# Kernel tuning notes

Hardware: AMD Instinct MI355X
Metric: run time of the kernel (lower is better)

## Reference

```python
import jax, jax.numpy as jnp
import numpy as np

N, G, MAX_N, E, H = 20000, 200, 100, 320000, 4
F_IN, NHID, NCLS = 128, 128, 10
DQ = 2 * NHID   # pooling-stack input dim = 2*nhid
K1 = 25         # ceil(0.25 * avg_num_nodes)


def _lin(key, fi, fo):
    kw, kb = jax.random.split(key)
    s = 1.0 / np.sqrt(fi)
    return (jax.random.uniform(kw, (fi, fo), jnp.float32, -s, s),
            jax.random.uniform(kb, (fo,), jnp.float32, -s, s))


def setup_inputs():
    key = jax.random.key(0)
    ks = jax.random.split(key, 32)
    x = jax.random.normal(ks[0], (N, F_IN), jnp.float32)
    gid = jax.random.randint(ks[1], (E,), 0, G)
    u = jax.random.randint(ks[2], (E,), 0, MAX_N)
    v = jax.random.randint(ks[3], (E,), 0, MAX_N)
    edge_index = jnp.stack([gid * MAX_N + u, gid * MAX_N + v]).astype(jnp.int32)
    batch = (jnp.arange(N) // MAX_N).astype(jnp.int32)
    d = {}
    d['x'], d['edge_index'], d['batch'] = x, edge_index, batch
    d['W1'], d['b1'] = _lin(ks[4], F_IN, NHID)
    d['W2'], d['b2'] = _lin(ks[5], NHID, NHID)
    d['S0'] = jax.random.normal(ks[6], (1, K1, DQ), jnp.float32) * (1.0 / np.sqrt(DQ))
    d['Wq0'], d['bq0'] = _lin(ks[7], DQ, DQ)
    d['Wk0'], d['bk0'] = _lin(ks[8], DQ, DQ)
    d['Wv0'], d['bv0'] = _lin(ks[9], DQ, DQ)
    d['Wo0'], d['bo0'] = _lin(ks[10], DQ, DQ)
    d['Wq1'], d['bq1'] = _lin(ks[11], DQ, NHID)
    d['Wk1'], d['bk1'] = _lin(ks[12], DQ, NHID)
    d['Wv1'], d['bv1'] = _lin(ks[13], DQ, NHID)
    d['Wo1'], d['bo1'] = _lin(ks[14], NHID, NHID)
    d['S2'] = jax.random.normal(ks[15], (1, 1, NHID), jnp.float32) * (1.0 / np.sqrt(NHID))
    d['Wq2'], d['bq2'] = _lin(ks[16], NHID, NHID)
    d['Wk2'], d['bk2'] = _lin(ks[17], NHID, NHID)
    d['Wv2'], d['bv2'] = _lin(ks[18], NHID, NHID)
    d['Wo2'], d['bo2'] = _lin(ks[19], NHID, NHID)
    d['Wl'], d['bl'] = _lin(ks[20], NHID, NHID)
    d['Wc1'], d['bc1'] = _lin(ks[21], NHID, NHID)
    d['Wc2'], d['bc2'] = _lin(ks[22], NHID, NHID // 2)
    d['Wc3'], d['bc3'] = _lin(ks[23], NHID // 2, NCLS)
    return d


def gcn(h, src, dst, W, b):
    # PyG GCNConv: add self loops, sym-normalize, scatter-add, bias
    h = h @ W
    loop = jnp.arange(N, dtype=src.dtype)
    s = jnp.concatenate([src, loop])
    t = jnp.concatenate([dst, loop])
    deg = jax.ops.segment_sum(jnp.ones(s.shape[0], h.dtype), t, num_segments=N)
    dinv = jax.lax.rsqrt(jnp.maximum(deg, 1.0))
    norm = (dinv[s] * dinv[t])[:, None]
    return jax.ops.segment_sum(h[s] * norm, t, num_segments=N) + b


def to_dense(v, batch):
    counts = jax.ops.segment_sum(jnp.ones(v.shape[0], jnp.int32), batch, num_segments=G)
    start = jnp.cumsum(counts) - counts
    pos = jnp.arange(v.shape[0]) - start[batch]
    dense = jnp.zeros((G, MAX_N, v.shape[1]), v.dtype).at[batch, pos].set(v)
    mask = jnp.zeros((G, MAX_N), bool).at[batch, pos].set(True)
    return dense, mask


def attn_block(Q, K, V, Wo, bo, mask_bias):
    # MAB core with cluster=True: softmax over the QUERY (seed) axis, ln=False
    B, nq, dv = Q.shape
    dh = dv // H
    Qh = Q.reshape(B, nq, H, dh)
    Kh = K.reshape(B, K.shape[1], H, dh)
    Vh = V.reshape(B, V.shape[1], H, dh)
    score = jnp.einsum('bqhd,bkhd->bhqk', Qh, Kh) / jnp.sqrt(jnp.float32(dv))
    if mask_bias is not None:
        score = score + mask_bias[:, None, None, :]
    A = jax.nn.softmax(score, axis=2)  # cluster assignment over seeds
    O = Q + jnp.einsum('bhqk,bkhd->bqhd', A, Vh).reshape(B, nq, dv)
    return O + jax.nn.relu(O @ Wo + bo)


def reference(x, edge_index, batch, W1, b1, W2, b2, S0, Wq0, bq0, Wk0, bk0, Wv0, bv0, Wo0, bo0,
              Wq1, bq1, Wk1, bk1, Wv1, bv1, Wo1, bo1, S2, Wq2, bq2, Wk2, bk2, Wv2, bv2, Wo2, bo2,
              Wl, bl, Wc1, bc1, Wc2, bc2, Wc3, bc3):
    src, dst = edge_index[0], edge_index[1]
    x1 = jax.nn.relu(gcn(x, src, dst, W1, b1))
    x2 = jax.nn.relu(gcn(x1, src, dst, W2, b2))
    p1 = jax.ops.segment_sum(x1, batch, num_segments=G)  # global_add_pool
    p2 = jax.ops.segment_sum(x2, batch, num_segments=G)
    xcat = jnp.concatenate([x1, x2], axis=1)             # [N, 2*nhid]
    dense, mask = to_dense(xcat, batch)
    mask_bias = (1.0 - mask.astype(jnp.float32)) * -1e9
    # --- GMPool_G: PMA with GCNConv for K/V on the node graph ---
    Kd, _ = to_dense(gcn(xcat, src, dst, Wk0, bk0), batch)
    Vd, _ = to_dense(gcn(xcat, src, dst, Wv0, bv0), batch)
    Q0 = jnp.broadcast_to(S0, (G, K1, DQ)) @ Wq0 + bq0
    O0 = attn_block(Q0, Kd, Vd, Wo0, bo0, mask_bias)     # [G, 25, 256]
    # --- SelfAtt (SAB), mask consumed above ---
    Q1 = O0 @ Wq1 + bq1
    K1d = O0 @ Wk1 + bk1
    V1d = O0 @ Wv1 + bv1
    O1 = attn_block(Q1, K1d, V1d, Wo1, bo1, None)        # [G, 25, 128]
    # --- GMPool_I: PMA with 1 seed ---
    Q2 = jnp.broadcast_to(S2, (G, 1, NHID)) @ Wq2 + bq2
    K2d = O1 @ Wk2 + bk2
    V2d = O1 @ Wv2 + bv2
    O2 = attn_block(Q2, K2d, V2d, Wo2, bo2, None)        # [G, 1, 128]
    z = (O2 @ Wl + bl)[:, 0, :]
    z = jax.nn.relu(z @ Wc1 + bc1)                        # dropout = identity at eval
    z = jax.nn.relu(z @ Wc2 + bc2)
    logits = z @ Wc3 + bc3
    return (logits, p1, p2)
```

## Files before the change

### kernel.cpp

```cpp
#include <hip/hip_runtime.h>
#include <hip/hip_bf16.h>
#include <cstdint>
#include <cstddef>

typedef __hip_bfloat16 bf16;
typedef __attribute__((ext_vector_type(8))) short s16x8;
typedef __attribute__((ext_vector_type(4))) float f32x4;

#define MAXN 100
#define HH   4
#define FIN  128
#define KS1  25

static inline int ceil_div(int a, int b){ return (a + b - 1) / b; }

__device__ inline short f2bf(float f){
  unsigned int u = __float_as_uint(f);
  u = (u + 0x7FFF + ((u >> 16) & 1)) >> 16;
  return (short)u;
}
__device__ inline float loadf(const void* s, int i, bool isbf){
  return isbf ? __bfloat162float(((const bf16*)s)[i]) : ((const float*)s)[i];
}
__device__ inline bool block_sniff(const void* x, int tid, int* flagS){
  if (tid < 64){
    unsigned short b = ((const unsigned short*)x)[2 * tid];
    float v = __uint_as_float(((unsigned)b) << 16);
    float a = fabsf(v);
    bool ok = (a >= 6.1e-5f && a <= 16384.f);
    unsigned long long m = __ballot(ok);
    if (tid == 0) *flagS = (__popcll(m) >= 32) ? 1 : 0;
  }
  __syncthreads();
  return *flagS != 0;
}

struct PrepBatch {
  const void* src[40];
  void*       dst[40];
  int         a[40];
  int         b[40];
  int         blk0[41];
  int         ne;
  const void* xptr;
};

__global__ __launch_bounds__(256) void prep_all(PrepBatch pb){
  __shared__ int flagS;
  int tid = threadIdx.x;
  bool isbf = block_sniff(pb.xptr, tid, &flagS);
  int blk = blockIdx.x;
  int t = 0;
  while (t + 1 < pb.ne && pb.blk0[t + 1] <= blk) t++;
  int local = blk - pb.blk0[t];
  const void* s = pb.src[t];
  int bt = pb.b[t];
  if (bt < 0){
    float val = (bt == -2) ? 1.0f : 0.0f;
    int n = pb.a[t];
    float* d = (float*)pb.dst[t];
    int v = local * 256 + tid;
    int base = v * 4;
    if (base + 3 < n) ((float4*)d)[v] = make_float4(val, val, val, val);
    else for (int j = base; j < n && j < base + 4; j++) d[j] = val;
  } else if (bt == 0){
    int n = pb.a[t];
    float* d = (float*)pb.dst[t];
    int v = local * 256 + tid;
    int base = v * 4;
    if (base + 3 < n){
      float4 f;
      if (isbf){
        ushort4 u = ((const ushort4*)s)[v];
        f.x = __uint_as_float(((unsigned)u.x) << 16);
        f.y = __uint_as_float(((unsigned)u.y) << 16);
        f.z = __uint_as_float(((unsigned)u.z) << 16);
        f.w = __uint_as_float(((unsigned)u.w) << 16);
      } else f = ((const float4*)s)[v];
      ((float4*)d)[v] = f;
    } else {
      for (int j = base; j < n && j < base + 4; j++) d[j] = loadf(s, j, isbf);
    }
  } else {
    int K = pb.a[t], Nn = bt, ldt = K + 8;
    short* d = (short*)pb.dst[t];
    int i = local * 256 + tid;
    if (i < K * Nn){
      int n = i / K, k = i - n * K;
      d[(size_t)n * ldt + k] = f2bf(loadf(s, (size_t)k * Nn + n, isbf));
    }
  }
}

__global__ __launch_bounds__(256) void adj_cnt(const int* __restrict__ src, const int* __restrict__ dst,
                                               float* __restrict__ A, int e){
  int i = blockIdx.x * 256 + threadIdx.x;
  if (i >= e) return;
  int s = src[i], d = dst[i];
  int g = d / MAXN;
  int dl = d - g * MAXN;
  int sl = s - (s / MAXN) * MAXN;
  atomicAdd(&A[(size_t)g * (MAXN * MAXN) + dl * MAXN + sl], 1.0f);
}

#define GLDK 136
__global__ __launch_bounds__(512) void gcn_all(
    const void* __restrict__ X,
    const float* __restrict__ Adj,
    const short* __restrict__ W1t, const float* __restrict__ b1,
    const short* __restrict__ W2t, const float* __restrict__ b2,
    short* __restrict__ xaggB,
    float* __restrict__ p1, float* __restrict__ p2)
{
  __shared__ short As[112 * GLDK];
  __shared__ short S1[112 * GLDK];
  __shared__ short S2[128 * GLDK];
  __shared__ short S4[128 * GLDK];
  __shared__ float dinvL[112];
  __shared__ int flagS;
  int g = blockIdx.x;
  int tid = threadIdx.x;
  bool isbf = block_sniff(X, tid, &flagS);
  int wave = tid >> 6, lane = tid & 63;
  int quad = lane >> 4, l16 = lane & 15;
  int gn = wave * 16 + l16;

  for (int i = tid; i < 112 * GLDK / 2; i += 512){ ((int*)As)[i] = 0; ((int*)S1)[i] = 0; }
  for (int i = tid; i < 128 * GLDK / 2; i += 512){ ((int*)S2)[i] = 0; ((int*)S4)[i] = 0; }

  const float* Ag = Adj + (size_t)g * (MAXN * MAXN);
  if (tid < 400){
    int r = tid >> 2, j0 = (tid & 3) * 25;
    const float* row = Ag + r * MAXN + j0;
    float s = 0.f;
#pragma unroll
    for (int j = 0; j < 25; j++) s += row[j];
    s += __shfl_xor(s, 1); s += __shfl_xor(s, 2);
    if ((tid & 3) == 0) dinvL[r] = rsqrtf(1.0f + s);
  }
  __syncthreads();

  for (int i = tid; i < MAXN * MAXN; i += 512){
    int r = i / MAXN, s = i - r * MAXN;
    float v = Ag[i] + (r == s ? 1.0f : 0.0f);
    As[r * GLDK + s] = f2bf(v * dinvL[r] * dinvL[s]);
  }
  for (int i = tid; i < MAXN * 16; i += 512){
    int r = i >> 4, k8 = (i & 15) << 3;
    s16x8 v;
    if (isbf){
      v = *reinterpret_cast<const s16x8*>((const short*)X + (size_t)(g * MAXN + r) * 128 + k8);
    } else {
      const float* ap = (const float*)X + (size_t)(g * MAXN + r) * 128 + k8;
      float4 f0 = *reinterpret_cast<const float4*>(ap);
      float4 f1 = *reinterpret_cast<const float4*>(ap + 4);
      v[0] = f2bf(f0.x); v[1] = f2bf(f0.y); v[2] = f2bf(f0.z); v[3] = f2bf(f0.w);
      v[4] = f2bf(f1.x); v[5] = f2bf(f1.y); v[6] = f2bf(f1.z); v[7] = f2bf(f1.w);
    }
    *reinterpret_cast<s16x8*>(&S1[r * GLDK + k8]) = v;
  }
  __syncthreads();

  f32x4 acc[7];
  auto zacc = [&](){
#pragma unroll
    for (int rt = 0; rt < 7; rt++) acc[rt] = (f32x4){0.f,0.f,0.f,0.f};
  };
  auto passL = [&](const short* Abuf, const short* Bbuf){
#pragma unroll
    for (int kt = 0; kt < 4; kt++){
      int kb = kt * 32 + quad * 8;
      s16x8 bf0 = *reinterpret_cast<const s16x8*>(&Bbuf[gn * GLDK + kb]);
#pragma unroll
      for (int rt = 0; rt < 7; rt++){
// ... 11 lines not shown
      for (int rt = 0; rt < 7; rt++){
        s16x8 a = *reinterpret_cast<const s16x8*>(&Abuf[(rt * 16 + l16) * GLDK + kb]);
        acc[rt] = __builtin_amdgcn_mfma_f32_16x16x32_bf16(a, bf0, acc[rt], 0, 0, 0);
      }
    }
  };
  auto writeB = [&](short* Bbuf){
#pragma unroll
    for (int rt = 0; rt < 7; rt++){
      short4 o;
      o.x = f2bf(acc[rt][0]); o.y = f2bf(acc[rt][1]);
      o.z = f2bf(acc[rt][2]); o.w = f2bf(acc[rt][3]);
      *reinterpret_cast<short4*>(&Bbuf[gn * GLDK + rt * 16 + quad * 4]) = o;
    }
  };

  float s1sum = 0.f, s2sum = 0.f;
  auto hopEpi = [&](const float* bias, short* AoutA, short* BoutB, float& sum){
    float bv = bias[gn];
#pragma unroll
    for (int rt = 0; rt < 7; rt++){
      float vals[4];
#pragma unroll
      for (int r = 0; r < 4; r++){
        int row = rt * 16 + quad * 4 + r;
        float v = fmaxf(acc[rt][r] + bv, 0.f);
        vals[r] = v;
        if (row < MAXN) sum += v;
      }
      short4 o;
      o.x = f2bf(vals[0]); o.y = f2bf(vals[1]); o.z = f2bf(vals[2]); o.w = f2bf(vals[3]);
      *reinterpret_cast<short4*>(&BoutB[gn * GLDK + rt * 16 + quad * 4]) = o;
      if (AoutA){
        AoutA[(rt * 16 + quad * 4 + 0) * GLDK + gn] = o.x;
        AoutA[(rt * 16 + quad * 4 + 1) * GLDK + gn] = o.y;
        AoutA[(rt * 16 + quad * 4 + 2) * GLDK + gn] = o.z;
        AoutA[(rt * 16 + quad * 4 + 3) * GLDK + gn] = o.w;
      }
    }
  };
  auto xaggEpi = [&](int colbase){
    int col = gn + colbase;
#pragma unroll
    for (int rt = 0; rt < 7; rt++){
#pragma unroll
      for (int r = 0; r < 4; r++){
        int row = rt * 16 + quad * 4 + r;
        if (row < MAXN) xaggB[(size_t)(g * MAXN + row) * 256 + col] = f2bf(acc[rt][r]);
      }
    }
  };

  zacc(); passG(S1, W1t); writeB(S2);
  __syncthreads();
  zacc(); passL(As, S2); hopEpi(b1, S1, S4, s1sum);
  __syncthreads();
  zacc(); passL(As, S4); xaggEpi(0);
  zacc(); passG(S1, W2t); writeB(S2);
  __syncthreads();
  zacc(); passL(As, S2); hopEpi(b2, nullptr, S4, s2sum);
  __syncthreads();
  zacc(); passL(As, S4); xaggEpi(128);

  s1sum += __shfl_xor(s1sum, 16); s1sum += __shfl_xor(s1sum, 32);
  s2sum += __shfl_xor(s2sum, 16); s2sum += __shfl_xor(s2sum, 32);
  if (quad == 0){
    p1[g * 128 + gn] = s1sum;
    p2[g * 128 + gn] = s2sum;
  }
}

__global__ __launch_bounds__(256) void ubar_q0(const float* __restrict__ S0,
    const float* __restrict__ Wq0, const float* __restrict__ bq0,
    const float* __restrict__ Wk0, const float* __restrict__ bk0,
    float* __restrict__ Q0, short* __restrict__ Ubart, float* __restrict__ cvec)
{
  __shared__ float q0s[64];
  int j = blockIdx.x, h = j / 25, q = j - h * 25;
  int tid = threadIdx.x;
  if (tid < 64){
    int c = h * 64 + tid;
    float acc = bq0[c];
    for (int e = 0; e < 256; e++) acc = fmaf(S0[q * 256 + e], Wq0[e * 256 + c], acc);
    q0s[tid] = acc;
    Q0[q * 256 + c] = acc;
  }
  __syncthreads();
  float acc = 0.f;
  const float* wp = &Wk0[(size_t)tid * 256 + h * 64];
#pragma unroll
  for (int d = 0; d < 64; d++) acc = fmaf(wp[d], q0s[d], acc);
  Ubart[(size_t)j * 264 + tid] = f2bf(acc * 0.0625f);
  if (tid == 0){
    float cb = 0.f;
    for (int d = 0; d < 64; d++) cb = fmaf(bk0[h * 64 + d], q0s[d], cb);
    cvec[j] = cb * 0.0625f;
  }
}

struct TailParams {
  const short* xaggB;
  const short* Wv0t;
  const short* Ubart;
  const float* biasVS;
  const float* Q0;
  const short* Wo0t;  const float* bo0;
  const short* WQKVt; const float* biasQKV;
  const short* Wo1t;  const float* bo1;
  const float *S2, *Wq2, *bq2, *Wv2, *bv2, *Wo2, *bo2, *Wl, *bl, *Wc1, *bc1, *Wc2, *bc2, *Wc3, *bc3;
  float* out;
};

__global__ __launch_bounds__(512) void tail_all(TailParams P)
{
  __shared__ __align__(16) char pool[162880];
  char*  R1   = pool;
  char*  R2   = pool + 57344;
  char*  R3   = pool + 97344;
  float* Ssh  = (float*)R2;
  short* Pbf  = (short*)R1;
  short* Abf  = (short*)(R1 + 34816);
  float* hva  = (float*)(R1 + 51712);
  float* hvb  = (float*)(R1 + 52224);
  float* O1F  = (float*)R1;
  float* OaF  = (float*)R2;
  float* ObF  = (float*)R2;
  short* Abf2 = (short*)(R2 + 26000);
  float* QKV  = (float*)R3;
  float* Ss2  = (float*)(R3 + 38800);
  float* hpart= (float*)(R3 + 38800);

  int g = blockIdx.x, tid = threadIdx.x;
  int wave = tid >> 6, lane = tid & 63, quad = lane >> 4, l16 = lane & 15;

  {
    const short* xa = P.xaggB + (size_t)g * MAXN * 256;
    for (int i = tid; i < 3200; i += 512){
      int r = i >> 5, ch = i & 31;
      s16x8 v = *reinterpret_cast<const s16x8*>(xa + r * 256 + ch * 8);
      int b = (r * 512 + ch * 16) ^ ((r & 7) << 4);
      *reinterpret_cast<s16x8*>(R1 + b) = v;
    }
    s16x8 z; 
#pragma unroll
    for (int j = 0; j < 8; j++) z[j] = 0;
    if (tid < 384){
      int r = 100 + (tid >> 5), ch = tid & 31;
      int b = (r * 512 + ch * 16) ^ ((r & 7) << 4);
      *reinterpret_cast<s16x8*>(R1 + b) = z;
    }
    {
      int c = tid >> 1, slot = tid & 1;
      int b = (c * 256 + 224 + slot * 16) ^ ((c & 7) << 4);
      *reinterpret_cast<s16x8*>(R3 + b) = z;
    }
  }
  __syncthreads();

  {
#pragma unroll
    for (int cg = 0; cg < 2; cg++){
      int c = wave * 32 + cg * 16 + l16;
      const short* bw = P.Wv0t + (size_t)c * 264;
      s16x8 B[8];
#pragma unroll
      for (int kt = 0; kt < 8; kt++) B[kt] = *reinterpret_cast<const s16x8*>(bw + kt * 32 + quad * 8);
      f32x4 acc[7];
#pragma unroll
      for (int rt = 0; rt < 7; rt++) acc[rt] = (f32x4){0.f,0.f,0.f,0.f};
#pragma unroll
      for (int kt = 0; kt < 8; kt++){
        int kb = kt * 32 + quad * 8;
#pragma unroll
        for (int rt = 0; rt < 7; rt++){
          int row = rt * 16 + l16;
          int ab = (row * 512 + kb * 2) ^ ((row & 7) << 4);
          s16x8 a = *reinterpret_cast<const s16x8*>(R1 + ab);
          acc[rt] = __builtin_amdgcn_mfma_f32_16x16x32_bf16(a, B[kt], acc[rt], 0, 0, 0);
        }
      }
      float bv = P.biasVS[c];
#pragma unroll
      for (int rt = 0; rt < 7; rt++){
        int node0 = rt * 16 + quad * 4;
        short4 o;
        o.x = f2bf(acc[rt][0] + bv); o.y = f2bf(acc[rt][1] + bv);
        o.z = f2bf(acc[rt][2] + bv); o.w = f2bf(acc[rt][3] + bv);
        int b = (c * 256 + node0 * 2) ^ ((c & 7) << 4);
        *reinterpret_cast<short4*>(R3 + b) = o;
      }
    }
    if (wave < 7){
      int j = wave * 16 + l16;
      const short* bw = P.Ubart + (size_t)j * 264;
      s16x8 B[8];
#pragma unroll
      for (int kt = 0; kt < 8; kt++) B[kt] = *reinterpret_cast<const s16x8*>(bw + kt * 32 + quad * 8);
      f32x4 acc[7];
#pragma unroll
      for (int rt = 0; rt < 7; rt++) acc[rt] = (f32x4){0.f,0.f,0.f,0.f};
#pragma unroll
      for (int kt = 0; kt < 8; kt++){
        int kb = kt * 32 + quad * 8;
#pragma unroll
        for (int rt = 0; rt < 7; rt++){
          int row = rt * 16 + l16;
          int ab = (row * 512 + kb * 2) ^ ((row & 7) << 4);
          s16x8 a = *reinterpret_cast<const s16x8*>(R1 + ab);
          acc[rt] = __builtin_amdgcn_mfma_f32_16x16x32_bf16(a, B[kt], acc[rt], 0, 0, 0);
        }
      }
      if (j < 100){
        float cv = P.biasVS[256 + j];
#pragma unroll
        for (int rt = 0; rt < 7; rt++){
#pragma unroll
          for (int r = 0; r < 4; r++){
            int node = rt * 16 + quad * 4 + r;
            if (node < MAXN) Ssh[node * 100 + j] = acc[rt][r] + cv;
          }
        }
      }
    }
  }
  __syncthreads();

  if (tid < 400){
    int k = tid >> 2, h = tid & 3;
    const float* base = &Ssh[k * 100 + h * 25];
    float v[25];
    float m = -1e30f;
#pragma unroll
    for (int q = 0; q < 25; q++){ v[q] = base[q]; m = fmaxf(m, v[q]); }
    float s = 0.f;
// ... 3 lines not shown
    short* pb = &Pbf[h * 32 * 136 + k];
#pragma unroll
    for (int q = 0; q < 25; q++) pb[q * 136] = f2bf(v[q] * inv);
  } else {
    for (int idx = tid - 400; idx < 1400; idx += 112){
      int r = idx / 14, c = idx - r * 14;
      int h = r / 25, q = r - h * 25;
      ((int*)Pbf)[(h * 32 + q) * 68 + 50 + c] = 0;
    }
  }
  __syncthreads();

  {
    int h = wave >> 1;
    int cbase = wave * 32;
    f32x4 acc[2][2];
#pragma unroll
    for (int rt = 0; rt < 2; rt++){ acc[rt][0] = (f32x4){0.f,0.f,0.f,0.f}; acc[rt][1] = acc[rt][0]; }
#pragma unroll
    for (int kt = 0; kt < 4; kt++){
      int kb = kt * 32 + quad * 8;
      int c0 = cbase + l16, c1 = cbase + 16 + l16;
      int b0 = (c0 * 256 + kb * 2) ^ ((c0 & 7) << 4);
      int b1 = (c1 * 256 + kb * 2) ^ ((c1 & 7) << 4);
      s16x8 vb0 = *reinterpret_cast<const s16x8*>(R3 + b0);
      s16x8 vb1 = *reinterpret_cast<const s16x8*>(R3 + b1);
#pragma unroll
      for (int rt = 0; rt < 2; rt++){
        s16x8 a = *reinterpret_cast<const s16x8*>(&Pbf[(h * 32 + rt * 16 + l16) * 136 + kb]);
        acc[rt][0] = __builtin_amdgcn_mfma_f32_16x16x32_bf16(a, vb0, acc[rt][0], 0, 0, 0);
        acc[rt][1] = __builtin_amdgcn_mfma_f32_16x16x32_bf16(a, vb1, acc[rt][1], 0, 0, 0);
      }
    }
#pragma unroll
    for (int cg = 0; cg < 2; cg++){
      int c = cbase + cg * 16 + l16;
#pragma unroll
      for (int rt = 0; rt < 2; rt++){
#pragma unroll
        for (int r = 0; r < 4; r++){
          int row = rt * 16 + quad * 4 + r;
          if (row < 25){
            float oa = acc[rt][cg][r] + P.Q0[row * 256 + c];
            OaF[row * 260 + c] = oa;
            Abf[row * 264 + c] = f2bf(oa);
          }
        }
      }
    }
  }
  __syncthreads();

  {
    int c0 = wave * 16 + l16, c1 = c0 + 128;
    s16x8 B0[8], B1[8];
#pragma unroll
    for (int kt = 0; kt < 8; kt++){
      int kb = kt * 32 + quad * 8;
// ... 32 lines not shown
      }
    }
  }
  __syncthreads();

  {
    int c0 = wave * 16 + l16;
    s16x8 B[3][8];
#pragma unroll
    for (int p2 = 0; p2 < 3; p2++)
#pragma unroll
      for (int kt = 0; kt < 8; kt++){
        int kb = kt * 32 + quad * 8;
        B[p2][kt] = *reinterpret_cast<const s16x8*>(&P.WQKVt[(size_t)(c0 + p2 * 128) * 264 + kb]);
      }
    f32x4 acc[3][2];
#pragma unroll
    for (int p2 = 0; p2 < 3; p2++)
#pragma unroll
      for (int rt = 0; rt < 2; rt++) acc[p2][rt] = (f32x4){0.f,0.f,0.f,0.f};
#pragma unroll
    for (int kt = 0; kt < 8; kt++){
      int kb = kt * 32 + quad * 8;
#pragma unroll
      for (int rt = 0; rt < 2; rt++){
        s16x8 a = *reinterpret_cast<const s16x8*>(&Abf[(rt * 16 + l16) * 264 + kb]);
#pragma unroll
        for (int p2 = 0; p2 < 3; p2++)
          acc[p2][rt] = __builtin_amdgcn_mfma_f32_16x16x32_bf16(a, B[p2][kt], acc[p2][rt], 0, 0, 0);
      }
    }
#pragma unroll
    for (int p2 = 0; p2 < 3; p2++){
      int col = c0 + p2 * 128;
      float bv = P.biasQKV[col];
#pragma unroll
      for (int rt = 0; rt < 2; rt++){
#pragma unroll
        for (int r = 0; r < 4; r++){
          int row = rt * 16 + quad * 4 + r;
          if (row < 25) QKV[row * 388 + col] = acc[p2][rt][r] + bv;
        }
      }
    }
  }
  __syncthreads();

  for (int idx = tid; idx < 2500; idx += 512){
    int h = idx / 625;
    int r = idx - h * 625;
    int q = r / 25, k = r - q * 25;
    const float* qp = &QKV[q * 388 + h * 32];
    const float* kp = &QKV[k * 388 + 128 + h * 32];
    float acc = 0.f;
#pragma unroll
    for (int d = 0; d < 32; d += 4){
      float4 a4 = *reinterpret_cast<const float4*>(&qp[d]);
      float4 b4 = *reinterpret_cast<const float4*>(&kp[d]);
      acc = fmaf(a4.x, b4.x, acc); acc = fmaf(a4.y, b4.y, acc);
      acc = fmaf(a4.z, b4.z, acc); acc = fmaf(a4.w, b4.w, acc);
    }
    Ss2[(h * 25 + q) * 26 + k] = acc * 0.0883883476f;
  }
  __syncthreads();
  if (tid < 100){
    int h = tid / 25, k = tid - h * 25;
    float m = -1e30f;
#pragma unroll
    for (int q = 0; q < 25; q++) m = fmaxf(m, Ss2[(h * 25 + q) * 26 + k]);
    float s = 0.f;
#pragma unroll
    for (int q = 0; q < 25; q++){ float e = __expf(Ss2[(h * 25 + q) * 26 + k] - m); Ss2[(h * 25 + q) * 26 + k] = e; s += e; }
    float inv = 1.0f / s;
#pragma unroll
    for (int q = 0; q < 25; q++) Ss2[(h * 25 + q) * 26 + k] *= inv;
  }
  __syncthreads();

  if (tid < 256){
    int qh = tid >> 7;
    int c = tid & 127, h = c >> 5;
    int q0 = qh * 13, nq = 13 - qh;
    float acc[13] = {};
    for (int k = 0; k < 25; k++){
      float v = QKV[k * 388 + 256 + c];
      for (int j = 0; j < nq; j++)
        acc[j] = fmaf(Ss2[(h * 25 + q0 + j) * 26 + k], v, acc[j]);
    }
    for (int j = 0; j < nq; j++){
      int q = q0 + j;
      float ob = QKV[q * 388 + c] + acc[j];
      ObF[q * 132 + c] = ob;
      Abf2[q * 136 + c] = f2bf(ob);
    }
  }
  __syncthreads();

  {
    int c0 = wave * 16 + l16;
    s16x8 B0[4];
#pragma unroll
    for (int kt = 0; kt < 4; kt++){
      int kb = kt * 32 + quad * 8;
      B0[kt] = *reinterpret_cast<const s16x8*>(&P.Wo1t[(size_t)c0 * 136 + kb]);
    }
    f32x4 a0 = (f32x4){0.f,0.f,0.f,0.f}, a1 = a0;
// ... 14 lines not shown
      if (row1 < 25){ float t = a1[r] + bv; O1F[row1 * 132 + c0] = ObF[row1 * 132 + c0] + fmaxf(t, 0.f); }
    }
  }
  __syncthreads();

  if (tid < 128){
    float s = 0.f;
    for (int k = 0; k < 25; k++) s += O1F[k * 132 + tid];
    hva[tid] = s;
  }
  __syncthreads();
  {
    int kh = tid >> 7, c = tid & 127, k0 = kh * 32;
    float s = 0.f;
    for (int k = k0; k < k0 + 32; k++)
      s = fmaf(P.S2[k], P.Wq2[k * 128 + c], fmaf(hva[k], P.Wv2[k * 128 + c], s));
    hpart[kh * 128 + c] = s;
    __syncthreads();
    if (tid < 128) hvb[c] = hpart[c] + hpart[128 + c] + hpart[256 + c] + hpart[384 + c]
                          + P.bq2[c] + 25.f * P.bv2[c];
    __syncthreads();
    s = 0.f;
    for (int k = k0; k < k0 + 32; k++) s = fmaf(hvb[k], P.Wo2[k * 128 + c], s);
    hpart[kh * 128 + c] = s;
    __syncthreads();
    if (tid < 128) hva[c] = hvb[c] + fmaxf(hpart[c] + hpart[128 + c] + hpart[256 + c] + hpart[384 + c] + P.bo2[c], 0.f);
    __syncthreads();
    s = 0.f;
    for (int k = k0; k < k0 + 32; k++) s = fmaf(hva[k], P.Wl[k * 128 + c], s);
    hpart[kh * 128 + c] = s;
    __syncthreads();
// ... 35 lines not shown
  const int E = in_sizes[1] / 2;
  const int G = N / MAXN;
  const int* srcp = edge;
  const int* dstp = edge + E;
  float* out = (float*)d_out;

  float* w = (float*)d_ws;
  size_t off = 0;
  auto alloc = [&](size_t nfl){ nfl = (nfl + 3) & ~(size_t)3; float* p = w + off; off += nfl; return p; };
  auto allocS = [&](size_t nsh)->short*{ size_t nfl = ((nsh + 1) / 2 + 3) & ~(size_t)3; short* p = (short*)(w + off); off += nfl; return p; };

  float* biasVS  = alloc(356);
  float* biasQKV = alloc(384);
  float* cvec = biasVS + 256;

  const int castT[24] = {4,6,7,8,9,10,11,15,23,24,25,26,29,30,31,32,33,34,35,36,37,38,39,40};
  float* wf[41] = {nullptr};
  for (int i = 0; i < 24; i++) wf[castT[i]] = alloc((size_t)in_sizes[castT[i]]);
  wf[13] = biasVS; wf[17] = biasQKV; wf[19] = biasQKV + 128; wf[21] = biasQKV + 256;

  float* Adj = alloc((size_t)G * MAXN * MAXN);
  float* Q0  = alloc(25 * 256);
  short* xaggB = allocS((size_t)N * 256);

  short* W1t   = allocS(128 * 136);
  short* W2t   = allocS(128 * 136);
  short* WVSt  = allocS(356 * 264);
  short* WQKVt = allocS(384 * 264);
  short* Wo0t  = allocS(256 * 264);
  short* Wo1t  = allocS(128 * 136);
  short* Ubart = WVSt + (size_t)256 * 264;
  if (off * sizeof(float) > ws_size) return;

  dim3 blk(256);

  PrepBatch pb; int ne = 0, blks = 0;
  pb.xptr = d_in[0];
  auto addC = [&](const void* s, float* d, int n){
    pb.src[ne]=s; pb.dst[ne]=d; pb.a[ne]=n; pb.b[ne]=0; pb.blk0[ne]=blks;
    blks += ceil_div(ceil_div(n, 4), 256); ne++; };
  auto addW = [&](const void* s, short* d, int K, int Nn){
    pb.src[ne]=s; pb.dst[ne]=d; pb.a[ne]=K; pb.b[ne]=Nn; pb.blk0[ne]=blks;
    blks += ceil_div(K * Nn, 256); ne++; };
  auto addF = [&](void* d, int n, int mode){
    pb.src[ne]=nullptr; pb.dst[ne]=d; pb.a[ne]=n; pb.b[ne]=mode; pb.blk0[ne]=blks;
    blks += ceil_div(ceil_div(n, 4), 256); ne++; };
  for (int i = 0; i < 24; i++){ int t = castT[i]; addC(d_in[t], wf[t], in_sizes[t]); }
  addC(d_in[13], biasVS, 256);
  addC(d_in[17], biasQKV, 128); addC(d_in[19], biasQKV + 128, 128); addC(d_in[21], biasQKV + 256, 128);
  addW(d_in[3],  W1t, 128, 128);             addW(d_in[5],  W2t, 128, 128);
  addW(d_in[12], WVSt, 256, 256);            addW(d_in[16], WQKVt, 256, 128);
  addW(d_in[18], WQKVt + 128*264, 256, 128); addW(d_in[20], WQKVt + 256*264, 256, 128);
  addW(d_in[14], Wo0t, 256, 256);            addW(d_in[22], Wo1t, 128, 128);
  addF(Adj, G * MAXN * MAXN, -1);
  pb.blk0[ne] = blks; pb.ne = ne;
  prep_all<<<dim3(blks), blk, 0, stream>>>(pb);

  adj_cnt<<<ceil_div(E, 256), blk, 0, stream>>>(srcp, dstp, Adj, E);

  gcn_all<<<dim3(G), dim3(512), 0, stream>>>(d_in[0], Adj, W1t, wf[4], W2t, wf[6],
                                             xaggB, out + 2000, out + 27600);

  ubar_q0<<<dim3(100), blk, 0, stream>>>(wf[7], wf[8], wf[9], wf[10], wf[11], Q0, Ubart, cvec);

  TailParams tp;
  tp.xaggB = xaggB; tp.Wv0t = WVSt; tp.Ubart = Ubart; tp.biasVS = biasVS;
  tp.Q0 = Q0;
  tp.Wo0t = Wo0t; tp.bo0 = wf[15];
  tp.WQKVt = WQKVt; tp.biasQKV = biasQKV;
  tp.Wo1t = Wo1t; tp.bo1 = wf[23];
  tp.S2 = wf[24]; tp.Wq2 = wf[25]; tp.bq2 = wf[26]; tp.Wv2 = wf[29]; tp.bv2 = wf[30];
  tp.Wo2 = wf[31]; tp.bo2 = wf[32]; tp.Wl = wf[33]; tp.bl = wf[34];
  tp.Wc1 = wf[35]; tp.bc1 = wf[36]; tp.Wc2 = wf[37]; tp.bc2 = wf[38];
  tp.Wc3 = wf[39]; tp.bc3 = wf[40];
  tp.out = out;
  tail_all<<<dim3(G), dim3(512), 0, stream>>>(tp);
}
```

Measured before the change: 241.6 us.

## Fuse GCN and tail kernels, fold edge counting and Ubar into prep

The GCN kernel and the attention tail kernel are merged into one per-graph kernel. The aggregated node features now go from registers straight into the swizzled shared-memory layout the tail reads, instead of making a bf16 round trip through global memory. The adjacency-count atomics and the Ubar/Q0 precompute become extra block ranges of the prep kernel, and the adjacency zero-fill moves to a hipMemsetAsync. This cuts the number of launches and drops a roughly 10 MB intermediate write and read. In exchange the fused kernel holds the large LDS pool and more live registers (the xag0 array) for the whole run, which may limit occupancy.

Result: slower. 259.5 us (+7.4%).

```diff
diff --git a/kernel.cpp b/kernel.cpp
--- a/kernel.cpp
+++ b/kernel.cpp
@@ -11,6 +11,7 @@
 #define HH   4
 #define FIN  128
 #define KS1  25
+#define GLDK 136
 
 static inline int ceil_div(int a, int b){ return (a + b - 1) / b; }
 
@@ -19,7 +20,7 @@
   u = (u + 0x7FFF + ((u >> 16) & 1)) >> 16;
   return (short)u;
 }
-__device__ inline float loadf(const void* s, int i, bool isbf){
+__device__ inline float loadf(const void* s, size_t i, bool isbf){
   return isbf ? __bfloat162float(((const bf16*)s)[i]) : ((const float*)s)[i];
 }
 __device__ inline bool block_sniff(const void* x, int tid, int* flagS){
@@ -43,27 +44,62 @@
   int         blk0[41];
   int         ne;
   const void* xptr;
+  const void *uS0, *uWq0, *ubq0, *uWk0, *ubk0;
+  float* uQ0; short* uUbart; float* ucvec;
+  const int *esrc, *edst; float* eadj; int ecnt;
+  int nUbar, nEdge;
 };
 
 __global__ __launch_bounds__(256) void prep_all(PrepBatch pb){
   __shared__ int flagS;
+  __shared__ float q0s[64];
   int tid = threadIdx.x;
   bool isbf = block_sniff(pb.xptr, tid, &flagS);
   int blk = blockIdx.x;
+
+  if (blk < pb.nUbar){
+    int j = blk, h = j / 25, q = j - h * 25;
+    if (tid < 64){
+      int c = h * 64 + tid;
+      float acc = loadf(pb.ubq0, c, isbf);
+      for (int e = 0; e < 256; e++)
+        acc = fmaf(loadf(pb.uS0, q * 256 + e, isbf), loadf(pb.uWq0, (size_t)e * 256 + c, isbf), acc);
+      q0s[tid] = acc;
+      pb.uQ0[q * 256 + c] = acc;
+    }
+    __syncthreads();
+    float acc = 0.f;
+    for (int d = 0; d < 64; d++)
+      acc = fmaf(loadf(pb.uWk0, (size_t)tid * 256 + h * 64 + d, isbf), q0s[d], acc);
+    pb.uUbart[(size_t)j * 264 + tid] = f2bf(acc * 0.0625f);
+    if (tid == 0){
+      float cb = 0.f;
+      for (int d = 0; d < 64; d++) cb = fmaf(loadf(pb.ubk0, h * 64 + d, isbf), q0s[d], cb);
+      pb.ucvec[j] = cb * 0.0625f;
+    }
+    return;
+  }
+  blk -= pb.nUbar;
+
+  if (blk < pb.nEdge){
+    int i = blk * 256 + tid;
+    if (i < pb.ecnt){
+      int s = pb.esrc[i], d = pb.edst[i];
+      int g = d / MAXN;
+      int dl = d - g * MAXN;
+      int sl = s - (s / MAXN) * MAXN;
+      atomicAdd(&pb.eadj[(size_t)g * (MAXN * MAXN) + dl * MAXN + sl], 1.0f);
+    }
+    return;
+  }
+  blk -= pb.nEdge;
+
   int t = 0;
   while (t + 1 < pb.ne && pb.blk0[t + 1] <= blk) t++;
   int local = blk - pb.blk0[t];
   const void* s = pb.src[t];
   int bt = pb.b[t];
-  if (bt < 0){
-    float val = (bt == -2) ? 1.0f : 0.0f;
-    int n = pb.a[t];
-    float* d = (float*)pb.dst[t];
-    int v = local * 256 + tid;
-    int base = v * 4;
-    if (base + 3 < n) ((float4*)d)[v] = make_float4(val, val, val, val);
-    else for (int j = base; j < n && j < base + 4; j++) d[j] = val;
-  } else if (bt == 0){
+  if (bt == 0){
     int n = pb.a[t];
     float* d = (float*)pb.dst[t];
     int v = local * 256 + tid;
@@ -92,43 +128,56 @@
   }
 }
 
-__global__ __launch_bounds__(256) void adj_cnt(const int* __restrict__ src, const int* __restrict__ dst,
-                                               float* __restrict__ A, int e){
-  int i = blockIdx.x * 256 + threadIdx.x;
-  if (i >= e) return;
-  int s = src[i], d = dst[i];
-  int g = d / MAXN;
-  int dl = d - g * MAXN;
-  int sl = s - (s / MAXN) * MAXN;
-  atomicAdd(&A[(size_t)g * (MAXN * MAXN) + dl * MAXN + sl], 1.0f);
-}
-
-#define GLDK 136
-__global__ __launch_bounds__(512) void gcn_all(
-    const void* __restrict__ X,
-    const float* __restrict__ Adj,
-    const short* __restrict__ W1t, const float* __restrict__ b1,
-    const short* __restrict__ W2t, const float* __restrict__ b2,
-    short* __restrict__ xaggB,
-    float* __restrict__ p1, float* __restrict__ p2)
+struct GTParams {
+  const void* X;
+  const float* Adj;
+  const short* W1t; const float* b1;
+  const short* W2t; const float* b2;
+  float* p1; float* p2;
+  const short* Wv0t;
+  const short* Ubart;
+  const float* biasVS;
+  const float* Q0;
+  const short* Wo0t;  const float* bo0;
+  const short* WQKVt; const float* biasQKV;
+  const short* Wo1t;  const float* bo1;
+  const float *S2w, *Wq2, *bq2, *Wv2, *bv2, *Wo2, *bo2, *Wl, *bl, *Wc1, *bc1, *Wc2, *bc2, *Wc3, *bc3;
+  float* out;
+};
+
+__global__ __launch_bounds__(512) void gcn_tail(GTParams P)
 {
-  __shared__ short As[112 * GLDK];
-  __shared__ short S1[112 * GLDK];
-  __shared__ short S2[128 * GLDK];
-  __shared__ short S4[128 * GLDK];
+  __shared__ __align__(16) char pool[162880];
   __shared__ float dinvL[112];
   __shared__ int flagS;
-  int g = blockIdx.x;
-  int tid = threadIdx.x;
-  bool isbf = block_sniff(X, tid, &flagS);
-  int wave = tid >> 6, lane = tid & 63;
-  int quad = lane >> 4, l16 = lane & 15;
+  short* S1x = (short*)(pool);
+  short* S2b = (short*)(pool + 30464);
+  short* S4b = (short*)(pool + 65280);
+  short* Asb = (short*)(pool + 100096);
+  char* R1 = pool;
+  char* RV = pool + 57344;
+  char* RS = pool + 122880;
+  float* Ssh  = (float*)RS;
+  short* Pbf  = (short*)R1;
+  short* Abf  = (short*)(R1 + 34816);
+  float* hva  = (float*)(R1 + 51712);
+  float* hvb  = (float*)(R1 + 52224);
+  float* O1F  = (float*)R1;
+  float* OaF  = (float*)RS;
+  float* ObF  = (float*)RS;
+  short* Abf2 = (short*)(RS + 26000);
+  float* QKV  = (float*)RV;
+  float* Ss2  = (float*)(RV + 38800);
+  float* hpart= (float*)(RV + 38800);
+
+  int g = blockIdx.x, tid = threadIdx.x;
+  bool isbf = block_sniff(P.X, tid, &flagS);
+  int wave = tid >> 6, lane = tid & 63, quad = lane >> 4, l16 = lane & 15;
   int gn = wave * 16 + l16;
 
-  for (int i = tid; i < 112 * GLDK / 2; i += 512){ ((int*)As)[i] = 0; ((int*)S1)[i] = 0; }
-  for (int i = tid; i < 128 * GLDK / 2; i += 512){ ((int*)S2)[i] = 0; ((int*)S4)[i] = 0; }
-
-  const float* Ag = Adj + (size_t)g * (MAXN * MAXN);
+  for (int i = tid; i < 162880 / 4; i += 512) ((int*)pool)[i] = 0;
+
+  const float* Ag = P.Adj + (size_t)g * (MAXN * MAXN);
   if (tid < 400){
     int r = tid >> 2, j0 = (tid & 3) * 25;
     const float* row = Ag + r * MAXN + j0;
@@ -143,21 +192,21 @@
   for (int i = tid; i < MAXN * MAXN; i += 512){
     int r = i / MAXN, s = i - r * MAXN;
     float v = Ag[i] + (r == s ? 1.0f : 0.0f);
-    As[r * GLDK + s] = f2bf(v * dinvL[r] * dinvL[s]);
+    Asb[r * GLDK + s] = f2bf(v * dinvL[r] * dinvL[s]);
   }
   for (int i = tid; i < MAXN * 16; i += 512){
     int r = i >> 4, k8 = (i & 15) << 3;
     s16x8 v;
     if (isbf){
-      v = *reinterpret_cast<const s16x8*>((const short*)X + (size_t)(g * MAXN + r) * 128 + k8);
+      v = *reinterpret_cast<const s16x8*>((const short*)P.X + (size_t)(g * MAXN + r) * 128 + k8);
     } else {
-      const float* ap = (const float*)X + (size_t)(g * MAXN + r) * 128 + k8;
+      const float* ap = (const float*)P.X + (size_t)(g * MAXN + r) * 128 + k8;
       float4 f0 = *reinterpret_cast<const float4*>(ap);
       float4 f1 = *reinterpret_cast<const float4*>(ap + 4);
       v[0] = f2bf(f0.x); v[1] = f2bf(f0.y); v[2] = f2bf(f0.z); v[3] = f2bf(f0.w);
       v[4] = f2bf(f1.x); v[5] = f2bf(f1.y); v[6] = f2bf(f1.z); v[7] = f2bf(f1.w);
     }
-    *reinterpret_cast<s16x8*>(&S1[r * GLDK + k8]) = v;
+    *reinterpret_cast<s16x8*>(&S1x[r * GLDK + k8]) = v;
   }
   __syncthreads();
 
@@ -199,7 +248,6 @@
       *reinterpret_cast<short4*>(&Bbuf[gn * GLDK + rt * 16 + quad * 4]) = o;
     }
   };
-
   float s1sum = 0.f, s2sum = 0.f;
   auto hopEpi = [&](const float* bias, short* AoutA, short* BoutB, float& sum){
     float bv = bias[gn];
@@ -224,121 +272,48 @@
       }
     }
   };
-  auto xaggEpi = [&](int colbase){
-    int col = gn + colbase;
-#pragma unroll
-    for (int rt = 0; rt < 7; rt++){
-#pragma unroll
-      for (int r = 0; r < 4; r++){
-        int row = rt * 16 + quad * 4 + r;
-        if (row < MAXN) xaggB[(size_t)(g * MAXN + row) * 256 + col] = f2bf(acc[rt][r]);
-      }
-    }
-  };
-
-  zacc(); passG(S1, W1t); writeB(S2);
-  __syncthreads();
-  zacc(); passL(As, S2); hopEpi(b1, S1, S4, s1sum);
-  __syncthreads();
-  zacc(); passL(As, S4); xaggEpi(0);
-  zacc(); passG(S1, W2t); writeB(S2);
-  __syncthreads();
-  zacc(); passL(As, S2); hopEpi(b2, nullptr, S4, s2sum);
-  __syncthreads();
-  zacc(); passL(As, S4); xaggEpi(128);
+
+  zacc(); passG(S1x, P.W1t); writeB(S2b);
+  __syncthreads();
+  zacc(); passL(Asb, S2b); hopEpi(P.b1, S1x, S4b, s1sum);
+  __syncthreads();
+  short4 xag0[7];
+  zacc(); passL(Asb, S4b);
+#pragma unroll
+  for (int rt = 0; rt < 7; rt++){
+    xag0[rt].x = f2bf(acc[rt][0]); xag0[rt].y = f2bf(acc[rt][1]);
+    xag0[rt].z = f2bf(acc[rt][2]); xag0[rt].w = f2bf(acc[rt][3]);
+  }
+  zacc(); passG(S1x, P.W2t); writeB(S2b);
+  __syncthreads();
+  zacc(); passL(Asb, S2b); hopEpi(P.b2, nullptr, S4b, s2sum);
+  __syncthreads();
+  zacc(); passL(Asb, S4b);
 
   s1sum += __shfl_xor(s1sum, 16); s1sum += __shfl_xor(s1sum, 32);
   s2sum += __shfl_xor(s2sum, 16); s2sum += __shfl_xor(s2sum, 32);
   if (quad == 0){
-    p1[g * 128 + gn] = s1sum;
-    p2[g * 128 + gn] = s2sum;
-  }
-}
-
-__global__ __launch_bounds__(256) void ubar_q0(const float* __restrict__ S0,
-    const float* __restrict__ Wq0, const float* __restrict__ bq0,
-    const float* __restrict__ Wk0, const float* __restrict__ bk0,
-    float* __restrict__ Q0, short* __restrict__ Ubart, float* __restrict__ cvec)
-{
-  __shared__ float q0s[64];
-  int j = blockIdx.x, h = j / 25, q = j - h * 25;
-  int tid = threadIdx.x;
-  if (tid < 64){
-    int c = h * 64 + tid;
-    float acc = bq0[c];
-    for (int e = 0; e < 256; e++) acc = fmaf(S0[q * 256 + e], Wq0[e * 256 + c], acc);
-    q0s[tid] = acc;
-    Q0[q * 256 + c] = acc;
-  }
-  __syncthreads();
-  float acc = 0.f;
-  const float* wp = &Wk0[(size_t)tid * 256 + h * 64];
-#pragma unroll
-  for (int d = 0; d < 64; d++) acc = fmaf(wp[d], q0s[d], acc);
-  Ubart[(size_t)j * 264 + tid] = f2bf(acc * 0.0625f);
-  if (tid == 0){
-    float cb = 0.f;
-    for (int d = 0; d < 64; d++) cb = fmaf(bk0[h * 64 + d], q0s[d], cb);
-    cvec[j] = cb * 0.0625f;
-  }
-}
-
-struct TailParams {
-  const short* xaggB;
-  const short* Wv0t;
-  const short* Ubart;
-  const float* biasVS;
-  const float* Q0;
-  const short* Wo0t;  const float* bo0;
-  const short* WQKVt; const float* biasQKV;
-  const short* Wo1t;  const float* bo1;
-  const float *S2, *Wq2, *bq2, *Wv2, *bv2, *Wo2, *bo2, *Wl, *bl, *Wc1, *bc1, *Wc2, *bc2, *Wc3, *bc3;
-  float* out;
-};
-
-__global__ __launch_bounds__(512) void tail_all(TailParams P)
-{
-  __shared__ __align__(16) char pool[162880];
-  char*  R1   = pool;
-  char*  R2   = pool + 57344;
-  char*  R3   = pool + 97344;
-  float* Ssh  = (float*)R2;
-  short* Pbf  = (short*)R1;
-  short* Abf  = (short*)(R1 + 34816);
-  float* hva  = (float*)(R1 + 51712);
-  float* hvb  = (float*)(R1 + 52224);
-  float* O1F  = (float*)R1;
-  float* OaF  = (float*)R2;
-  float* ObF  = (float*)R2;
-  short* Abf2 = (short*)(R2 + 26000);
-  float* QKV  = (float*)R3;
-  float* Ss2  = (float*)(R3 + 38800);
-  float* hpart= (float*)(R3 + 38800);
-
-  int g = blockIdx.x, tid = threadIdx.x;
-  int wave = tid >> 6, lane = tid & 63, quad = lane >> 4, l16 = lane & 15;
+    P.p1[g * 128 + gn] = s1sum;
+    P.p2[g * 128 + gn] = s2sum;
+  }
+  __syncthreads();
 
   {
-    const short* xa = P.xaggB + (size_t)g * MAXN * 256;
-    for (int i = tid; i < 3200; i += 512){
-      int r = i >> 5, ch = i & 31;
-      s16x8 v = *reinterpret_cast<const s16x8*>(xa + r * 256 + ch * 8);
-      int b = (r * 512 + ch * 16) ^ ((r & 7) << 4);
-      *reinterpret_cast<s16x8*>(R1 + b) = v;
-    }
-    s16x8 z; 
-#pragma unroll
-    for (int j = 0; j < 8; j++) z[j] = 0;
-    if (tid < 384){
-      int r = 100 + (tid >> 5), ch = tid & 31;
-      int b = (r * 512 + ch * 16) ^ ((r & 7) << 4);
-      *reinterpret_cast<s16x8*>(R1 + b) = z;
-    }
-    {
-      int c = tid >> 1, slot = tid & 1;
-      int b = (c * 256 + 224 + slot * 16) ^ ((c & 7) << 4);
-      *reinterpret_cast<s16x8*>(R3 + b) = z;
-    }
+    short v0[4];
+#pragma unroll
+    for (int rt = 0; rt < 7; rt++){
+      v0[0] = xag0[rt].x; v0[1] = xag0[rt].y; v0[2] = xag0[rt].z; v0[3] = xag0[rt].w;
+#pragma unroll
+      for (int r = 0; r < 4; r++){
+        int node = rt * 16 + quad * 4 + r;
+        if (node < MAXN){
+          int sw = (node & 7) << 4;
+          *(short*)(R1 + ((node * 512 + gn * 2) ^ sw)) = v0[r];
+          *(short*)(R1 + ((node * 512 + (gn + 128) * 2) ^ sw)) = f2bf(acc[rt][r]);
+        }
+      }
+    }
+    for (int i = tid; i < 1536; i += 512) ((int*)(R1 + 51200))[i] = 0;
   }
   __syncthreads();
 
@@ -350,9 +325,9 @@
       s16x8 B[8];
 #pragma unroll
       for (int kt = 0; kt < 8; kt++) B[kt] = *reinterpret_cast<const s16x8*>(bw + kt * 32 + quad * 8);
-      f32x4 acc[7];
-#pragma unroll
-      for (int rt = 0; rt < 7; rt++) acc[rt] = (f32x4){0.f,0.f,0.f,0.f};
+      f32x4 vac[7];
+#pragma unroll
+      for (int rt = 0; rt < 7; rt++) vac[rt] = (f32x4){0.f,0.f,0.f,0.f};
 #pragma unroll
       for (int kt = 0; kt < 8; kt++){
         int kb = kt * 32 + quad * 8;
@@ -361,7 +336,7 @@
           int row = rt * 16 + l16;
           int ab = (row * 512 + kb * 2) ^ ((row & 7) << 4);
           s16x8 a = *reinterpret_cast<const s16x8*>(R1 + ab);
-          acc[rt] = __builtin_amdgcn_mfma_f32_16x16x32_bf16(a, B[kt], acc[rt], 0, 0, 0);
+          vac[rt] = __builtin_amdgcn_mfma_f32_16x16x32_bf16(a, B[kt], vac[rt], 0, 0, 0);
         }
       }
       float bv = P.biasVS[c];
@@ -369,10 +344,10 @@
       for (int rt = 0; rt < 7; rt++){
         int node0 = rt * 16 + quad * 4;
         short4 o;
-        o.x = f2bf(acc[rt][0] + bv); o.y = f2bf(acc[rt][1] + bv);
-        o.z = f2bf(acc[rt][2] + bv); o.w = f2bf(acc[rt][3] + bv);
+        o.x = f2bf(vac[rt][0] + bv); o.y = f2bf(vac[rt][1] + bv);
+        o.z = f2bf(vac[rt][2] + bv); o.w = f2bf(vac[rt][3] + bv);
         int b = (c * 256 + node0 * 2) ^ ((c & 7) << 4);
-        *reinterpret_cast<short4*>(R3 + b) = o;
+        *reinterpret_cast<short4*>(RV + b) = o;
       }
     }
     if (wave < 7){
@@ -381,9 +356,9 @@
       s16x8 B[8];
 #pragma unroll
       for (int kt = 0; kt < 8; kt++) B[kt] = *reinterpret_cast<const s16x8*>(bw + kt * 32 + quad * 8);
-      f32x4 acc[7];
-#pragma unroll
-      for (int rt = 0; rt < 7; rt++) acc[rt] = (f32x4){0.f,0.f,0.f,0.f};
+      f32x4 sac[7];
+#pragma unroll
+      for (int rt = 0; rt < 7; rt++) sac[rt] = (f32x4){0.f,0.f,0.f,0.f};
 #pragma unroll
       for (int kt = 0; kt < 8; kt++){
         int kb = kt * 32 + quad * 8;
@@ -392,7 +367,7 @@
           int row = rt * 16 + l16;
           int ab = (row * 512 + kb * 2) ^ ((row & 7) << 4);
           s16x8 a = *reinterpret_cast<const s16x8*>(R1 + ab);
-          acc[rt] = __builtin_amdgcn_mfma_f32_16x16x32_bf16(a, B[kt], acc[rt], 0, 0, 0);
+          sac[rt] = __builtin_amdgcn_mfma_f32_16x16x32_bf16(a, B[kt], sac[rt], 0, 0, 0);
         }
       }
       if (j < 100){
@@ -402,7 +377,7 @@
 #pragma unroll
           for (int r = 0; r < 4; r++){
             int node = rt * 16 + quad * 4 + r;
-            if (node < MAXN) Ssh[node * 100 + j] = acc[rt][r] + cv;
+            if (node < MAXN) Ssh[node * 100 + j] = sac[rt][r] + cv;
           }
         }
       }
@@ -436,22 +411,22 @@
   {
     int h = wave >> 1;
     int cbase = wave * 32;
-    f32x4 acc[2][2];
-#pragma unroll
-    for (int rt = 0; rt < 2; rt++){ acc[rt][0] = (f32x4){0.f,0.f,0.f,0.f}; acc[rt][1] = acc[rt][0]; }
+    f32x4 aac[2][2];
+#pragma unroll
+    for (int rt = 0; rt < 2; rt++){ aac[rt][0] = (f32x4){0.f,0.f,0.f,0.f}; aac[rt][1] = aac[rt][0]; }
 #pragma unroll
     for (int kt = 0; kt < 4; kt++){
       int kb = kt * 32 + quad * 8;
       int c0 = cbase + l16, c1 = cbase + 16 + l16;
       int b0 = (c0 * 256 + kb * 2) ^ ((c0 & 7) << 4);
       int b1 = (c1 * 256 + kb * 2) ^ ((c1 & 7) << 4);
-      s16x8 vb0 = *reinterpret_cast<const s16x8*>(R3 + b0);
-      s16x8 vb1 = *reinterpret_cast<const s16x8*>(R3 + b1);
+      s16x8 vb0 = *reinterpret_cast<const s16x8*>(RV + b0);
+      s16x8 vb1 = *reinterpret_cast<const s16x8*>(RV + b1);
 #pragma unroll
       for (int rt = 0; rt < 2; rt++){
         s16x8 a = *reinterpret_cast<const s16x8*>(&Pbf[(h * 32 + rt * 16 + l16) * 136 + kb]);
-        acc[rt][0] = __builtin_amdgcn_mfma_f32_16x16x32_bf16(a, vb0, acc[rt][0], 0, 0, 0);
-        acc[rt][1] = __builtin_amdgcn_mfma_f32_16x16x32_bf16(a, vb1, acc[rt][1], 0, 0, 0);
+        aac[rt][0] = __builtin_amdgcn_mfma_f32_16x16x32_bf16(a, vb0, aac[rt][0], 0, 0, 0);
+        aac[rt][1] = __builtin_amdgcn_mfma_f32_16x16x32_bf16(a, vb1, aac[rt][1], 0, 0, 0);
       }
     }
 #pragma unroll
@@ -463,7 +438,7 @@
         for (int r = 0; r < 4; r++){
           int row = rt * 16 + quad * 4 + r;
           if (row < 25){
-            float oa = acc[rt][cg][r] + P.Q0[row * 256 + c];
+            float oa = aac[rt][cg][r] + P.Q0[row * 256 + c];
             OaF[row * 260 + c] = oa;
             Abf[row * 264 + c] = f2bf(oa);
           }
@@ -526,11 +501,11 @@
         int kb = kt * 32 + quad * 8;
         B[p2][kt] = *reinterpret_cast<const s16x8*>(&P.WQKVt[(size_t)(c0 + p2 * 128) * 264 + kb]);
       }
-    f32x4 acc[3][2];
+    f32x4 qac[3][2];
 #pragma unroll
     for (int p2 = 0; p2 < 3; p2++)
 #pragma unroll
-      for (int rt = 0; rt < 2; rt++) acc[p2][rt] = (f32x4){0.f,0.f,0.f,0.f};
+      for (int rt = 0; rt < 2; rt++) qac[p2][rt] = (f32x4){0.f,0.f,0.f,0.f};
 #pragma unroll
     for (int kt = 0; kt < 8; kt++){
       int kb = kt * 32 + quad * 8;
@@ -539,7 +514,7 @@
         s16x8 a = *reinterpret_cast<const s16x8*>(&Abf[(rt * 16 + l16) * 264 + kb]);
 #pragma unroll
         for (int p2 = 0; p2 < 3; p2++)
-          acc[p2][rt] = __builtin_amdgcn_mfma_f32_16x16x32_bf16(a, B[p2][kt], acc[p2][rt], 0, 0, 0);
+          qac[p2][rt] = __builtin_amdgcn_mfma_f32_16x16x32_bf16(a, B[p2][kt], qac[p2][rt], 0, 0, 0);
       }
     }
 #pragma unroll
@@ -551,7 +526,7 @@
 #pragma unroll
         for (int r = 0; r < 4; r++){
           int row = rt * 16 + quad * 4 + r;
-          if (row < 25) QKV[row * 388 + col] = acc[p2][rt][r] + bv;
+          if (row < 25) QKV[row * 388 + col] = qac[p2][rt][r] + bv;
         }
       }
     }
@@ -564,15 +539,15 @@
     int q = r / 25, k = r - q * 25;
     const float* qp = &QKV[q * 388 + h * 32];
     const float* kp = &QKV[k * 388 + 128 + h * 32];
-    float acc = 0.f;
+    float sac = 0.f;
 #pragma unroll
     for (int d = 0; d < 32; d += 4){
       float4 a4 = *reinterpret_cast<const float4*>(&qp[d]);
       float4 b4 = *reinterpret_cast<const float4*>(&kp[d]);
-      acc = fmaf(a4.x, b4.x, acc); acc = fmaf(a4.y, b4.y, acc);
-      acc = fmaf(a4.z, b4.z, acc); acc = fmaf(a4.w, b4.w, acc);
-    }
-    Ss2[(h * 25 + q) * 26 + k] = acc * 0.0883883476f;
+      sac = fmaf(a4.x, b4.x, sac); sac = fmaf(a4.y, b4.y, sac);
+      sac = fmaf(a4.z, b4.z, sac); sac = fmaf(a4.w, b4.w, sac);
+    }
+    Ss2[(h * 25 + q) * 26 + k] = sac * 0.0883883476f;
   }
   __syncthreads();
   if (tid < 100){
@@ -593,15 +568,15 @@
     int qh = tid >> 7;
     int c = tid & 127, h = c >> 5;
     int q0 = qh * 13, nq = 13 - qh;
-    float acc[13] = {};
+    float oac[13] = {};
     for (int k = 0; k < 25; k++){
       float v = QKV[k * 388 + 256 + c];
       for (int j = 0; j < nq; j++)
-        acc[j] = fmaf(Ss2[(h * 25 + q0 + j) * 26 + k], v, acc[j]);
+        oac[j] = fmaf(Ss2[(h * 25 + q0 + j) * 26 + k], v, oac[j]);
     }
     for (int j = 0; j < nq; j++){
       int q = q0 + j;
-      float ob = QKV[q * 388 + c] + acc[j];
+      float ob = QKV[q * 388 + c] + oac[j];
       ObF[q * 132 + c] = ob;
       Abf2[q * 136 + c] = f2bf(ob);
     }
@@ -646,7 +621,7 @@
     int kh = tid >> 7, c = tid & 127, k0 = kh * 32;
     float s = 0.f;
     for (int k = k0; k < k0 + 32; k++)
-      s = fmaf(P.S2[k], P.Wq2[k * 128 + c], fmaf(hva[k], P.Wv2[k * 128 + c], s));
+      s = fmaf(P.S2w[k], P.Wq2[k * 128 + c], fmaf(hva[k], P.Wv2[k * 128 + c], s));
     hpart[kh * 128 + c] = s;
     __syncthreads();
     if (tid < 128) hvb[c] = hpart[c] + hpart[128 + c] + hpart[256 + c] + hpart[384 + c]
@@ -712,14 +687,13 @@
   float* biasQKV = alloc(384);
   float* cvec = biasVS + 256;
 
-  const int castT[24] = {4,6,7,8,9,10,11,15,23,24,25,26,29,30,31,32,33,34,35,36,37,38,39,40};
+  const int castT[19] = {4,6,15,23,24,25,26,29,30,31,32,33,34,35,36,37,38,39,40};
   float* wf[41] = {nullptr};
-  for (int i = 0; i < 24; i++) wf[castT[i]] = alloc((size_t)in_sizes[castT[i]]);
+  for (int i = 0; i < 19; i++) wf[castT[i]] = alloc((size_t)in_sizes[castT[i]]);
   wf[13] = biasVS; wf[17] = biasQKV; wf[19] = biasQKV + 128; wf[21] = biasQKV + 256;
 
   float* Adj = alloc((size_t)G * MAXN * MAXN);
   float* Q0  = alloc(25 * 256);
-  short* xaggB = allocS((size_t)N * 256);
 
   short* W1t   = allocS(128 * 136);
   short* W2t   = allocS(128 * 136);
@@ -732,45 +706,43 @@
 
   dim3 blk(256);
 
+  (void)hipMemsetAsync(Adj, 0, (size_t)G * MAXN * MAXN * sizeof(float), stream);
+
   PrepBatch pb; int ne = 0, blks = 0;
   pb.xptr = d_in[0];
+  pb.uS0 = d_in[7]; pb.uWq0 = d_in[8]; pb.ubq0 = d_in[9]; pb.uWk0 = d_in[10]; pb.ubk0 = d_in[11];
+  pb.uQ0 = Q0; pb.uUbart = Ubart; pb.ucvec = cvec;
+  pb.esrc = srcp; pb.edst = dstp; pb.eadj = Adj; pb.ecnt = E;
+  pb.nUbar = 100; pb.nEdge = ceil_div(E, 256);
   auto addC = [&](const void* s, float* d, int n){
     pb.src[ne]=s; pb.dst[ne]=d; pb.a[ne]=n; pb.b[ne]=0; pb.blk0[ne]=blks;
     blks += ceil_div(ceil_div(n, 4), 256); ne++; };
   auto addW = [&](const void* s, short* d, int K, int Nn){
     pb.src[ne]=s; pb.dst[ne]=d; pb.a[ne]=K; pb.b[ne]=Nn; pb.blk0[ne]=blks;
     blks += ceil_div(K * Nn, 256); ne++; };
-  auto addF = [&](void* d, int n, int mode){
-    pb.src[ne]=nullptr; pb.dst[ne]=d; pb.a[ne]=n; pb.b[ne]=mode; pb.blk0[ne]=blks;
-    blks += ceil_div(ceil_div(n, 4), 256); ne++; };
-  for (int i = 0; i < 24; i++){ int t = castT[i]; addC(d_in[t], wf[t], in_sizes[t]); }
+  for (int i = 0; i < 19; i++){ int t = castT[i]; addC(d_in[t], wf[t], in_sizes[t]); }
   addC(d_in[13], biasVS, 256);
   addC(d_in[17], biasQKV, 128); addC(d_in[19], biasQKV + 128, 128); addC(d_in[21], biasQKV + 256, 128);
   addW(d_in[3],  W1t, 128, 128);             addW(d_in[5],  W2t, 128, 128);
   addW(d_in[12], WVSt, 256, 256);            addW(d_in[16], WQKVt, 256, 128);
   addW(d_in[18], WQKVt + 128*264, 256, 128); addW(d_in[20], WQKVt + 256*264, 256, 128);
   addW(d_in[14], Wo0t, 256, 256);            addW(d_in[22], Wo1t, 128, 128);
-  addF(Adj, G * MAXN * MAXN, -1);
   pb.blk0[ne] = blks; pb.ne = ne;
-  prep_all<<<dim3(blks), blk, 0, stream>>>(pb);
-
-  adj_cnt<<<ceil_div(E, 256), blk, 0, stream>>>(srcp, dstp, Adj, E);
-
-  gcn_all<<<dim3(G), dim3(512), 0, stream>>>(d_in[0], Adj, W1t, wf[4], W2t, wf[6],
-                                             xaggB, out + 2000, out + 27600);
-
-  ubar_q0<<<dim3(100), blk, 0, stream>>>(wf[7], wf[8], wf[9], wf[10], wf[11], Q0, Ubart, cvec);
-
-  TailParams tp;
-  tp.xaggB = xaggB; tp.Wv0t = WVSt; tp.Ubart = Ubart; tp.biasVS = biasVS;
+  prep_all<<<dim3(pb.nUbar + pb.nEdge + blks), blk, 0, stream>>>(pb);
+
+  GTParams tp;
+  tp.X = d_in[0]; tp.Adj = Adj;
+  tp.W1t = W1t; tp.b1 = wf[4]; tp.W2t = W2t; tp.b2 = wf[6];
+  tp.p1 = out + 2000; tp.p2 = out + 27600;
+  tp.Wv0t = WVSt; tp.Ubart = Ubart; tp.biasVS = biasVS;
   tp.Q0 = Q0;
   tp.Wo0t = Wo0t; tp.bo0 = wf[15];
   tp.WQKVt = WQKVt; tp.biasQKV = biasQKV;
   tp.Wo1t = Wo1t; tp.bo1 = wf[23];
-  tp.S2 = wf[24]; tp.Wq2 = wf[25]; tp.bq2 = wf[26]; tp.Wv2 = wf[29]; tp.bv2 = wf[30];
+  tp.S2w = wf[24]; tp.Wq2 = wf[25]; tp.bq2 = wf[26]; tp.Wv2 = wf[29]; tp.bv2 = wf[30];
   tp.Wo2 = wf[31]; tp.bo2 = wf[32]; tp.Wl = wf[33]; tp.bl = wf[34];
   tp.Wc1 = wf[35]; tp.bc1 = wf[36]; tp.Wc2 = wf[37]; tp.bc2 = wf[38];
   tp.Wc3 = wf[39]; tp.bc3 = wf[40];
   tp.out = out;
-  tail_all<<<dim3(G), dim3(512), 0, stream>>>(tp);
+  gcn_tail<<<dim3(G), dim3(512), 0, stream>>>(tp);
 }
```
